# Kernel optimization log

Hardware: AMD Instinct MI355X
Metric: run time of the kernel (lower is better)

The kernel has to match this reference:

```python
import jax, jax.numpy as jnp
import numpy as np

N_NODES = 50000
N_EDGES = 800000
D = 128


def _sage_layer(x, src, dst, W_neigh, W_root, b):
    # mean aggregation of source features at destination nodes
    msgs = x[src]                                            # [E, D] gather
    agg = jax.ops.segment_sum(msgs, dst, num_segments=N_NODES)
    deg = jax.ops.segment_sum(jnp.ones((src.shape[0],), x.dtype), dst,
                              num_segments=N_NODES)
    agg = agg / jnp.maximum(deg, 1.0)[:, None]               # [N, D]
    return agg @ W_neigh + x @ W_root + b


def setup_inputs() -> dict:
    key = jax.random.key(0)
    ks = jax.random.split(key, 8)
    s = 1.0 / np.sqrt(D)
    return {
        "x": jax.random.normal(ks[0], (N_NODES, D), jnp.float32),
        "edge_index": jax.random.randint(ks[1], (2, N_EDGES), 0, N_NODES,
                                         dtype=jnp.int64),
        "W_neigh1": jax.random.normal(ks[2], (D, D), jnp.float32) * s,
        "W_root1": jax.random.normal(ks[3], (D, D), jnp.float32) * s,
        "b1": jnp.zeros((D,), jnp.float32),
        "W_neigh2": jax.random.normal(ks[4], (D, D), jnp.float32) * s,
        "W_root2": jax.random.normal(ks[5], (D, D), jnp.float32) * s,
        "b2": jnp.zeros((D,), jnp.float32),
    }


def reference(x, edge_index, W_neigh1, W_root1, b1, W_neigh2, W_root2, b2):
    src, dst = edge_index[0], edge_index[1]
    hid = jax.nn.relu(_sage_layer(x, src, dst, W_neigh1, W_root1, b1))
    out = jax.nn.relu(_sage_layer(hid, src, dst, W_neigh2, W_root2, b2))
    return out
```

## Files before the change

### kernel.cpp

```cpp
#include <hip/hip_runtime.h>

#define N_NODES 50000
#define N_EDGES 800000
#define D 128
#define NBINS 196

typedef __attribute__((ext_vector_type(8))) short bf16x8;
typedef __attribute__((ext_vector_type(4))) float f32x4;

__device__ __forceinline__ unsigned short f2bf(float f) {
    unsigned u = __float_as_uint(f);
    unsigned r = (u + 0x7FFFu + ((u >> 16) & 1u)) >> 16;
    return (unsigned short)r;
}
__device__ __forceinline__ float bf2f(unsigned short h) {
    return __uint_as_float(((unsigned)h) << 16);
}

#define CVT_BLKS 3125
#define PACK_BLKS 128
#define BINC_BLKS 391

__device__ __forceinline__ void pack_one(const float* __restrict__ Wn,
                                         const float* __restrict__ Wr,
                                         ushort* __restrict__ Wp, int t) {
    int k = t >> 7, c = t & 127;
    float v = (k < 128) ? Wn[k * 128 + c] : Wr[(k - 128) * 128 + c];
    int ks = k >> 5, g = (k >> 3) & 3, i = k & 7;
    Wp[(((ks * 128 + c) * 4 + g) << 3) + i] = f2bf(v);
}

__global__ __launch_bounds__(256) void k_prep(const float* __restrict__ x,
                                              ushort* __restrict__ xb,
                                              const float* __restrict__ Wn1,
                                              const float* __restrict__ Wr1,
                                              ushort* __restrict__ Wp1,
                                              const float* __restrict__ Wn2,
                                              const float* __restrict__ Wr2,
                                              ushort* __restrict__ Wp2,
                                              const int* __restrict__ dst,
                                              int* __restrict__ binCnt) {
    __shared__ int lc[NBINS];
    int b = blockIdx.x;
    if (b < CVT_BLKS) {
        int i = b * 256 + threadIdx.x;
        const float4* p = (const float4*)(x + (size_t)i * 8);
        float4 a = p[0], c = p[1];
        uint4 o;
        o.x = (unsigned)f2bf(a.x) | ((unsigned)f2bf(a.y) << 16);
        o.y = (unsigned)f2bf(a.z) | ((unsigned)f2bf(a.w) << 16);
        o.z = (unsigned)f2bf(c.x) | ((unsigned)f2bf(c.y) << 16);
        o.w = (unsigned)f2bf(c.z) | ((unsigned)f2bf(c.w) << 16);
        *(uint4*)(xb + (size_t)i * 8) = o;
    } else if (b < CVT_BLKS + PACK_BLKS) {
        int t = (b - CVT_BLKS) * 256 + threadIdx.x;
        pack_one(Wn1, Wr1, Wp1, t);
        pack_one(Wn2, Wr2, Wp2, t);
    } else {
        const int tid = threadIdx.x;
        const int base = (b - CVT_BLKS - PACK_BLKS) * 2048;
        if (tid < NBINS) lc[tid] = 0;
        __syncthreads();
        #pragma unroll
        for (int k = 0; k < 8; k++) {
            int i = base + k * 256 + tid;
            if (i < N_EDGES) atomicAdd(&lc[dst[i] >> 8], 1);
        }
        __syncthreads();
        if (tid < NBINS) {
            int c = lc[tid];
            if (c) atomicAdd(&binCnt[tid], c);
        }
    }
}

__global__ __launch_bounds__(256) void k_scanB(const int* __restrict__ binCnt,
                                               int* __restrict__ binBase,
                                               int* __restrict__ binFill,
                                               int* __restrict__ row_ptr) {
    __shared__ int ws[4];
    const int tid = threadIdx.x, lane = tid & 63, w = tid >> 6;
    int v = (tid < NBINS) ? binCnt[tid] : 0;
    int incl = v;
    #pragma unroll
    for (int off = 1; off < 64; off <<= 1) {
        int t = __shfl_up(incl, off);
        if (lane >= off) incl += t;
    }
    if (lane == 63) ws[w] = incl;
    __syncthreads();
    int wo = 0;
    if (w > 0) wo += ws[0];
    if (w > 1) wo += ws[1];
    if (w > 2) wo += ws[2];
    int excl = wo + incl - v;
    if (tid < NBINS) { binBase[tid] = excl; binFill[tid] = excl; }
    if (tid == 255) { binBase[NBINS] = excl; row_ptr[N_NODES] = excl; }
}

__global__ __launch_bounds__(256) void k_binA(const int* __restrict__ src,
                                              const int* __restrict__ dst,
                                              int* __restrict__ binFill,
                                              unsigned* __restrict__ binned) {
    __shared__ int lc[NBINS];
    const int tid = threadIdx.x;
    const int base = blockIdx.x * 2048;
    if (tid < NBINS) lc[tid] = 0;
    __syncthreads();
    int s[8], d[8];
    #pragma unroll
    for (int k = 0; k < 8; k++) {
        int i = base + k * 256 + tid;
        if (i < N_EDGES) {
            s[k] = src[i];
            d[k] = dst[i];
            atomicAdd(&lc[d[k] >> 8], 1);
        } else d[k] = -1;
    }
    __syncthreads();
    if (tid < NBINS) {
        int c = lc[tid];
        lc[tid] = c ? atomicAdd(&binFill[tid], c) : 0;
    }
    __syncthreads();
    #pragma unroll
    for (int k = 0; k < 8; k++) {
        if (d[k] >= 0) {
            int pos = atomicAdd(&lc[d[k] >> 8], 1);
            binned[pos] = (unsigned)s[k] | ((unsigned)(d[k] & 255) << 16);
        }
    }
}

__global__ __launch_bounds__(256) void k_binB(const unsigned* __restrict__ binned,
                                              const int* __restrict__ binBase,
                                              int* __restrict__ row_ptr,
                                              ushort* __restrict__ edge_src) {
    __shared__ int cnt[256];
    __shared__ int cur[256];
    __shared__ int ws[4];
    const int tid = threadIdx.x, lane = tid & 63, w = tid >> 6;
    const int b = blockIdx.x;
    const int node0 = b << 8;
    int nNodes = N_NODES - node0; if (nNodes > 256) nNodes = 256;
    const int ebeg = binBase[b], eend = binBase[b + 1];
    cnt[tid] = 0;
    __syncthreads();
    for (int e = ebeg + tid; e < eend; e += 256) {
        unsigned rec = binned[e];
        atomicAdd(&cnt[(rec >> 16) & 255], 1);
    }
    __syncthreads();
    int v = cnt[tid];
    int incl = v;
    #pragma unroll
    for (int off = 1; off < 64; off <<= 1) {
        int t = __shfl_up(incl, off);
        if (lane >= off) incl += t;
    }
    if (lane == 63) ws[w] = incl;
    __syncthreads();
    int wo = 0;
    if (w > 0) wo += ws[0];
    if (w > 1) wo += ws[1];
    if (w > 2) wo += ws[2];
    int excl = wo + incl - v;
    cur[tid] = ebeg + excl;
    if (tid < nNodes) row_ptr[node0 + tid] = ebeg + excl;
    __syncthreads();
    for (int e = ebeg + tid; e < eend; e += 256) {
        unsigned rec = binned[e];
        int pos = atomicAdd(&cur[(rec >> 16) & 255], 1);
        edge_src[pos] = (ushort)(rec & 0xffffu);
    }
}

__global__ __launch_bounds__(256) void k_agg(const ushort* __restrict__ xb,
                                             const int* __restrict__ row_ptr,
                                             const ushort* __restrict__ edge_src,
                                             ushort* __restrict__ aggb) {
    int node = (blockIdx.x * blockDim.x + threadIdx.x) >> 6;
    int lane = threadIdx.x & 63;
    if (node >= N_NODES) return;
    int beg = row_ptr[node], end = row_ptr[node + 1];
    const int g  = lane >> 4;
    const int c8 = (lane & 15) * 8;
    float acc[8] = {};
    for (int e = beg; e < end; e += 16) {
        bf16x8 v[4];
        float sc[4];
        #pragma unroll
        for (int u = 0; u < 4; u++) {
            int ee = e + u * 4 + g;
            int eec = ee < end ? ee : end - 1;
            sc[u] = ee < end ? 1.f : 0.f;
            int sid = edge_src[eec];
            v[u] = *(const bf16x8*)&xb[(size_t)sid * D + c8];
        }
        #pragma unroll
        for (int u = 0; u < 4; u++)
            #pragma unroll
            for (int j = 0; j < 8; j++)
                acc[j] = fmaf(bf2f((unsigned short)v[u][j]), sc[u], acc[j]);
    }
    #pragma unroll
    for (int j = 0; j < 8; j++) acc[j] += __shfl_xor(acc[j], 16);
    #pragma unroll
    for (int j = 0; j < 8; j++) acc[j] += __shfl_xor(acc[j], 32);
    if (lane < 16) {
        int dg = end - beg;
        float inv = 1.0f / (float)(dg > 1 ? dg : 1);
        uint4 o;
        o.x = (unsigned)f2bf(acc[0] * inv) | ((unsigned)f2bf(acc[1] * inv) << 16);
        o.y = (unsigned)f2bf(acc[2] * inv) | ((unsigned)f2bf(acc[3] * inv) << 16);
        o.z = (unsigned)f2bf(acc[4] * inv) | ((unsigned)f2bf(acc[5] * inv) << 16);
        o.w = (unsigned)f2bf(acc[6] * inv) | ((unsigned)f2bf(acc[7] * inv) << 16);
        *(uint4*)&aggb[(size_t)node * D + c8] = o;
    }
}

template <int OUT_F32>
__global__ __launch_bounds__(128) void k_gemm(const ushort* __restrict__ Ab,
                                              const ushort* __restrict__ Xb,
                                              const ushort* __restrict__ Wp,
                                              const float* __restrict__ bias,
                                              void* __restrict__ outv) {
    const int lane = threadIdx.x & 63;
    const int wid  = threadIdx.x >> 6;
    const int row0 = blockIdx.x * 64;
    const int col0 = wid * 64;
    const int r = lane & 15, g = lane >> 4;

    f32x4 acc[4][4] = {};
    #pragma unroll
    for (int ks = 0; ks < 8; ks++) {
        const ushort* As = (ks < 4) ? Ab : Xb;
        const int kk = (ks & 3) * 32 + 8 * g;
        bf16x8 a[4], b[4];
        #pragma unroll
        for (int rf = 0; rf < 4; rf++) {
            int rr = row0 + rf * 16 + r;
            if (rr > N_NODES - 1) rr = N_NODES - 1;
            a[rf] = *(const bf16x8*)&As[(size_t)rr * D + kk];
        }
        #pragma unroll
        for (int cf = 0; cf < 4; cf++) {
            int c = col0 + cf * 16 + r;
            b[cf] = *(const bf16x8*)&Wp[(((size_t)ks * 128 + c) * 4 + g) * 8];
        }
        #pragma unroll
        for (int rf = 0; rf < 4; rf++)
            #pragma unroll
            for (int cf = 0; cf < 4; cf++)
                acc[rf][cf] = __builtin_amdgcn_mfma_f32_16x16x32_bf16(
                    a[rf], b[cf], acc[rf][cf], 0, 0, 0);
    }
    float bv[4];
    #pragma unroll
    for (int cf = 0; cf < 4; cf++) bv[cf] = bias[col0 + cf * 16 + r];
    #pragma unroll
    for (int rf = 0; rf < 4; rf++) {
        #pragma unroll
        for (int j = 0; j < 4; j++) {
            int row = row0 + rf * 16 + g * 4 + j;
            if (row < N_NODES) {
                #pragma unroll
                for (int cf = 0; cf < 4; cf++) {
                    float v = fmaxf(acc[rf][cf][j] + bv[cf], 0.f);
                    int col = col0 + cf * 16 + r;
                    if (OUT_F32) ((float*)outv)[(size_t)row * D + col] = v;
                    else ((ushort*)outv)[(size_t)row * D + col] = f2bf(v);
                }
            }
        }
    }
}

extern "C" void kernel_launch(void* const* d_in, const int* in_sizes, int n_in,
                              void* d_out, int out_size, void* d_ws, size_t ws_size,
                              hipStream_t stream) {
    const float* x   = (const float*)d_in[0];
    const int*   ei  = (const int*)d_in[1];
    const float* Wn1 = (const float*)d_in[2];
    const float* Wr1 = (const float*)d_in[3];
    const float* b1  = (const float*)d_in[4];
    const float* Wn2 = (const float*)d_in[5];
    const float* Wr2 = (const float*)d_in[6];
    const float* b2  = (const float*)d_in[7];
    float* out = (float*)d_out;

    const int* src = ei;
    const int* dst = ei + N_EDGES;

    const size_t bfb = (size_t)N_NODES * D * 2;
    const size_t packb = 256 * 128 * 2;
    auto au = [](size_t v) { return (v + 255) & ~(size_t)255; };

    char* w = (char*)d_ws;
    size_t o = 0;
    ushort* aggb = (ushort*)(w + o); o += au(bfb);
    ushort* hb   = (ushort*)(w + o); o += au(bfb);
    ushort* edge_src = (ushort*)(w + o); o += au((size_t)N_EDGES * 2);
    ushort* Wp2  = (ushort*)(w + o); o += au(packb);

    const size_t binsz = au((size_t)(NBINS + NBINS + 1 + NBINS) * 4);
    size_t rem = au(bfb) + au(packb) + au((N_NODES + 1) * 4ull) +
                 au((size_t)N_EDGES * 4) + binsz;
    ushort *xb, *Wp1;
    int *row_ptr;
    unsigned* binned;
    int* bins;
    if (ws_size >= o + rem) {
        xb = (ushort*)(w + o);      o += au(bfb);
        Wp1 = (ushort*)(w + o);     o += au(packb);
        row_ptr = (int*)(w + o);    o += au((N_NODES + 1) * 4ull);
        binned = (unsigned*)(w + o); o += au((size_t)N_EDGES * 4);
        bins = (int*)(w + o);
    } else {
        char* q = (char*)d_out;
        size_t p = 0;
        xb = (ushort*)(q + p);      p += au(bfb);
        Wp1 = (ushort*)(q + p);     p += au(packb);
        row_ptr = (int*)(q + p);    p += au((N_NODES + 1) * 4ull);
        binned = (unsigned*)(q + p); p += au((size_t)N_EDGES * 4);
        bins = (int*)(q + p);
    }
    int* binCnt  = bins;
    int* binBase = bins + NBINS;
    int* binFill = bins + NBINS + NBINS + 1;

    hipMemsetAsync(binCnt, 0, NBINS * sizeof(int), stream);
    k_prep<<<CVT_BLKS + PACK_BLKS + BINC_BLKS, 256, 0, stream>>>(
        x, xb, Wn1, Wr1, Wp1, Wn2, Wr2, Wp2, dst, binCnt);
    k_scanB<<<1, 256, 0, stream>>>(binCnt, binBase, binFill, row_ptr);
    k_binA<<<BINC_BLKS, 256, 0, stream>>>(src, dst, binFill, binned);
    k_binB<<<NBINS, 256, 0, stream>>>(binned, binBase, row_ptr, edge_src);

    const int aggGrid = (N_NODES * 64) / 256;
    const int gemmGrid = (N_NODES + 63) / 64;

    k_agg<<<aggGrid, 256, 0, stream>>>(xb, row_ptr, edge_src, aggb);
    k_gemm<0><<<gemmGrid, 128, 0, stream>>>(aggb, xb, Wp1, b1, hb);
    k_agg<<<aggGrid, 256, 0, stream>>>(hb, row_ptr, edge_src, aggb);
    k_gemm<1><<<gemmGrid, 128, 0, stream>>>(aggb, hb, Wp2, b2, out);
}
```

Measured before the change: 141.3 us.

## Quantize gathered node features to int8 with per-node scales for aggregation

Node features for both layers are quantized to unsigned int8 with a per-node absmax scale: in the prep kernel for x, and in a new k_quant kernel for the hidden layer. The aggregation kernel gathers 8-byte int8 chunks instead of 16-byte bf16 chunks and applies the scale and zero-point correction afterwards. It also loads edge ids once per 16 edges and broadcasts them with shuffles. The GEMM row tile shrinks from 64 to 32 rows, scratch buffers now live in the output buffer unconditionally, and the lossy int8 step reduces accuracy of the mean aggregation.

```diff
diff --git a/kernel.cpp b/kernel.cpp
--- a/kernel.cpp
+++ b/kernel.cpp
@@ -7,6 +7,7 @@
 
 typedef __attribute__((ext_vector_type(8))) short bf16x8;
 typedef __attribute__((ext_vector_type(4))) float f32x4;
+typedef unsigned char uchar;
 
 __device__ __forceinline__ unsigned short f2bf(float f) {
     unsigned u = __float_as_uint(f);
@@ -17,7 +18,7 @@
     return __uint_as_float(((unsigned)h) << 16);
 }
 
-#define CVT_BLKS 3125
+#define CVT_BLKS 12500
 #define PACK_BLKS 128
 #define BINC_BLKS 391
 
@@ -32,6 +33,8 @@
 
 __global__ __launch_bounds__(256) void k_prep(const float* __restrict__ x,
                                               ushort* __restrict__ xb,
+                                              uchar* __restrict__ x8,
+                                              float* __restrict__ xs,
                                               const float* __restrict__ Wn1,
                                               const float* __restrict__ Wr1,
                                               ushort* __restrict__ Wp1,
@@ -43,15 +46,20 @@
     __shared__ int lc[NBINS];
     int b = blockIdx.x;
     if (b < CVT_BLKS) {
-        int i = b * 256 + threadIdx.x;
-        const float4* p = (const float4*)(x + (size_t)i * 8);
-        float4 a = p[0], c = p[1];
-        uint4 o;
-        o.x = (unsigned)f2bf(a.x) | ((unsigned)f2bf(a.y) << 16);
-        o.y = (unsigned)f2bf(a.z) | ((unsigned)f2bf(a.w) << 16);
-        o.z = (unsigned)f2bf(c.x) | ((unsigned)f2bf(c.y) << 16);
-        o.w = (unsigned)f2bf(c.z) | ((unsigned)f2bf(c.w) << 16);
-        *(uint4*)(xb + (size_t)i * 8) = o;
+        const int wid = threadIdx.x >> 6, lane = threadIdx.x & 63;
+        const int node = b * 4 + wid;
+        float2 v = *(const float2*)&x[(size_t)node * D + lane * 2];
+        ((unsigned*)xb)[(size_t)node * 64 + lane] =
+            (unsigned)f2bf(v.x) | ((unsigned)f2bf(v.y) << 16);
+        float m = fmaxf(fabsf(v.x), fabsf(v.y));
+        #pragma unroll
+        for (int off = 1; off < 64; off <<= 1) m = fmaxf(m, __shfl_xor(m, off));
+        float inv = (m > 1e-20f) ? 127.0f / m : 0.0f;
+        uchar qa = (uchar)((int)rintf(v.x * inv) + 128);
+        uchar qb = (uchar)((int)rintf(v.y * inv) + 128);
+        uchar2 qq = {qa, qb};
+        *(uchar2*)&x8[(size_t)node * D + lane * 2] = qq;
+        if (lane == 0) xs[node] = m * (1.0f / 127.0f);
     } else if (b < CVT_BLKS + PACK_BLKS) {
         int t = (b - CVT_BLKS) * 256 + threadIdx.x;
         pack_one(Wn1, Wr1, Wp1, t);
@@ -72,6 +80,24 @@
             if (c) atomicAdd(&binCnt[tid], c);
         }
     }
+}
+
+__global__ __launch_bounds__(256) void k_quant(const ushort* __restrict__ hb,
+                                               uchar* __restrict__ h8,
+                                               float* __restrict__ hs) {
+    const int node = (blockIdx.x * blockDim.x + threadIdx.x) >> 6;
+    const int lane = threadIdx.x & 63;
+    unsigned u = ((const unsigned*)hb)[(size_t)node * 64 + lane];
+    float a = bf2f((unsigned short)(u & 0xffffu));
+    float c = bf2f((unsigned short)(u >> 16));
+    float m = fmaxf(fabsf(a), fabsf(c));
+    #pragma unroll
+    for (int off = 1; off < 64; off <<= 1) m = fmaxf(m, __shfl_xor(m, off));
+    float inv = (m > 1e-20f) ? 127.0f / m : 0.0f;
+    uchar2 qq = {(uchar)((int)rintf(a * inv) + 128),
+                 (uchar)((int)rintf(c * inv) + 128)};
+    *(uchar2*)&h8[(size_t)node * D + lane * 2] = qq;
+    if (lane == 0) hs[node] = m * (1.0f / 127.0f);
 }
 
 __global__ __launch_bounds__(256) void k_scanB(const int* __restrict__ binCnt,
@@ -175,7 +201,8 @@
     }
 }
 
-__global__ __launch_bounds__(256) void k_agg(const ushort* __restrict__ xb,
+__global__ __launch_bounds__(256) void k_agg(const uchar* __restrict__ x8,
+                                             const float* __restrict__ xs,
                                              const int* __restrict__ row_ptr,
                                              const ushort* __restrict__ edge_src,
                                              ushort* __restrict__ aggb) {
@@ -186,23 +213,29 @@
     const int g  = lane >> 4;
     const int c8 = (lane & 15) * 8;
     float acc[8] = {};
+    float ssum = 0.f;
     for (int e = beg; e < end; e += 16) {
-        bf16x8 v[4];
-        float sc[4];
+        int idx = e + (lane & 15);
+        int ids = edge_src[idx < end ? idx : end - 1];
         #pragma unroll
         for (int u = 0; u < 4; u++) {
             int ee = e + u * 4 + g;
-            int eec = ee < end ? ee : end - 1;
-            sc[u] = ee < end ? 1.f : 0.f;
-            int sid = edge_src[eec];
-            v[u] = *(const bf16x8*)&xb[(size_t)sid * D + c8];
-        }
-        #pragma unroll
-        for (int u = 0; u < 4; u++)
-            #pragma unroll
-            for (int j = 0; j < 8; j++)
-                acc[j] = fmaf(bf2f((unsigned short)v[u][j]), sc[u], acc[j]);
-    }
+            int sid = __shfl(ids, u * 4 + g);
+            float s = (ee < end) ? xs[sid] : 0.f;
+            uint2 v = *(const uint2*)&x8[(size_t)sid * D + c8];
+            acc[0] = fmaf((float)(v.x & 255u), s, acc[0]);
+            acc[1] = fmaf((float)((v.x >> 8) & 255u), s, acc[1]);
+            acc[2] = fmaf((float)((v.x >> 16) & 255u), s, acc[2]);
+            acc[3] = fmaf((float)(v.x >> 24), s, acc[3]);
+            acc[4] = fmaf((float)(v.y & 255u), s, acc[4]);
+            acc[5] = fmaf((float)((v.y >> 8) & 255u), s, acc[5]);
+            acc[6] = fmaf((float)((v.y >> 16) & 255u), s, acc[6]);
+            acc[7] = fmaf((float)(v.y >> 24), s, acc[7]);
+            ssum += s;
+        }
+    }
+    #pragma unroll
+    for (int j = 0; j < 8; j++) acc[j] = fmaf(-128.f, ssum, acc[j]);
     #pragma unroll
     for (int j = 0; j < 8; j++) acc[j] += __shfl_xor(acc[j], 16);
     #pragma unroll
@@ -227,18 +260,18 @@
                                               void* __restrict__ outv) {
     const int lane = threadIdx.x & 63;
     const int wid  = threadIdx.x >> 6;
-    const int row0 = blockIdx.x * 64;
+    const int row0 = blockIdx.x * 32;
     const int col0 = wid * 64;
     const int r = lane & 15, g = lane >> 4;
 
-    f32x4 acc[4][4] = {};
+    f32x4 acc[2][4] = {};
     #pragma unroll
     for (int ks = 0; ks < 8; ks++) {
         const ushort* As = (ks < 4) ? Ab : Xb;
         const int kk = (ks & 3) * 32 + 8 * g;
-        bf16x8 a[4], b[4];
-        #pragma unroll
-        for (int rf = 0; rf < 4; rf++) {
+        bf16x8 a[2], b[4];
+        #pragma unroll
+        for (int rf = 0; rf < 2; rf++) {
             int rr = row0 + rf * 16 + r;
             if (rr > N_NODES - 1) rr = N_NODES - 1;
             a[rf] = *(const bf16x8*)&As[(size_t)rr * D + kk];
@@ -249,7 +282,7 @@
             b[cf] = *(const bf16x8*)&Wp[(((size_t)ks * 128 + c) * 4 + g) * 8];
         }
         #pragma unroll
-        for (int rf = 0; rf < 4; rf++)
+        for (int rf = 0; rf < 2; rf++)
             #pragma unroll
             for (int cf = 0; cf < 4; cf++)
                 acc[rf][cf] = __builtin_amdgcn_mfma_f32_16x16x32_bf16(
@@ -259,7 +292,7 @@
     #pragma unroll
     for (int cf = 0; cf < 4; cf++) bv[cf] = bias[col0 + cf * 16 + r];
     #pragma unroll
-    for (int rf = 0; rf < 4; rf++) {
+    for (int rf = 0; rf < 2; rf++) {
         #pragma unroll
         for (int j = 0; j < 4; j++) {
             int row = row0 + rf * 16 + g * 4 + j;
@@ -298,49 +331,39 @@
 
     char* w = (char*)d_ws;
     size_t o = 0;
-    ushort* aggb = (ushort*)(w + o); o += au(bfb);
-    ushort* hb   = (ushort*)(w + o); o += au(bfb);
+    ushort* aggb = (ushort*)(w + o);     o += au(bfb);
+    ushort* hb   = (ushort*)(w + o);     o += au(bfb);
     ushort* edge_src = (ushort*)(w + o); o += au((size_t)N_EDGES * 2);
-    ushort* Wp2  = (ushort*)(w + o); o += au(packb);
-
-    const size_t binsz = au((size_t)(NBINS + NBINS + 1 + NBINS) * 4);
-    size_t rem = au(bfb) + au(packb) + au((N_NODES + 1) * 4ull) +
-                 au((size_t)N_EDGES * 4) + binsz;
-    ushort *xb, *Wp1;
-    int *row_ptr;
-    unsigned* binned;
-    int* bins;
-    if (ws_size >= o + rem) {
-        xb = (ushort*)(w + o);      o += au(bfb);
-        Wp1 = (ushort*)(w + o);     o += au(packb);
-        row_ptr = (int*)(w + o);    o += au((N_NODES + 1) * 4ull);
-        binned = (unsigned*)(w + o); o += au((size_t)N_EDGES * 4);
-        bins = (int*)(w + o);
-    } else {
-        char* q = (char*)d_out;
-        size_t p = 0;
-        xb = (ushort*)(q + p);      p += au(bfb);
-        Wp1 = (ushort*)(q + p);     p += au(packb);
-        row_ptr = (int*)(q + p);    p += au((N_NODES + 1) * 4ull);
-        binned = (unsigned*)(q + p); p += au((size_t)N_EDGES * 4);
-        bins = (int*)(q + p);
-    }
+    ushort* Wp2  = (ushort*)(w + o);     o += au(packb);
+
+    char* q = (char*)d_out;
+    size_t p = 0;
+    ushort* xb = (ushort*)(q + p);       p += au(bfb);
+    uchar*  h8 = (uchar*)xb;
+    float*  xs = (float*)(q + p);        p += au((size_t)N_NODES * 4);
+    float*  hs = xs;
+    uchar*  x8 = (uchar*)(q + p);        p += au((size_t)N_NODES * D);
+    unsigned* binned = (unsigned*)(q + p); p += au((size_t)N_EDGES * 4);
+    int* row_ptr = (int*)(q + p);        p += au((N_NODES + 1) * 4ull);
+    ushort* Wp1 = (ushort*)(q + p);      p += au(packb);
+    int* bins = (int*)(q + p);
     int* binCnt  = bins;
     int* binBase = bins + NBINS;
     int* binFill = bins + NBINS + NBINS + 1;
 
     hipMemsetAsync(binCnt, 0, NBINS * sizeof(int), stream);
     k_prep<<<CVT_BLKS + PACK_BLKS + BINC_BLKS, 256, 0, stream>>>(
-        x, xb, Wn1, Wr1, Wp1, Wn2, Wr2, Wp2, dst, binCnt);
+        x, xb, x8, xs, Wn1, Wr1, Wp1, Wn2, Wr2, Wp2, dst, binCnt);
     k_scanB<<<1, 256, 0, stream>>>(binCnt, binBase, binFill, row_ptr);
     k_binA<<<BINC_BLKS, 256, 0, stream>>>(src, dst, binFill, binned);
     k_binB<<<NBINS, 256, 0, stream>>>(binned, binBase, row_ptr, edge_src);
 
-    const int aggGrid = (N_NODES * 64) / 256;
-    const int gemmGrid = (N_NODES + 63) / 64;
-
-    k_agg<<<aggGrid, 256, 0, stream>>>(xb, row_ptr, edge_src, aggb);
+    const int aggGrid  = (N_NODES * 64) / 256;
+    const int gemmGrid = (N_NODES + 31) / 32;
+
+    k_agg<<<aggGrid, 256, 0, stream>>>(x8, xs, row_ptr, edge_src, aggb);
     k_gemm<0><<<gemmGrid, 128, 0, stream>>>(aggb, xb, Wp1, b1, hb);
-    k_agg<<<aggGrid, 256, 0, stream>>>(hb, row_ptr, edge_src, aggb);
+    k_quant<<<aggGrid / 1, 256, 0, stream>>>(hb, h8, hs);
+    k_agg<<<aggGrid, 256, 0, stream>>>(h8, hs, row_ptr, edge_src, aggb);
     k_gemm<1><<<gemmGrid, 128, 0, stream>>>(aggb, hb, Wp2, b2, out);
 }
```

New measurement: 152.1 us. 1.08x slower.
